# Performance work log

Measured on AMD Instinct MI355X. Metric: run time of the kernel, lower is better.

Reference implementation:

```python
import jax, jax.numpy as jnp
import numpy as np
import math

H = 8  # num_heads

def _gelu(x):
    return jax.nn.gelu(x, approximate=False)

def setup_inputs() -> dict:
    key = jax.random.key(0)
    ks = jax.random.split(key, 16)
    B, N, T, D = 2, 16, 127, 128
    s = 0.02
    inp = {}
    inp["padded_batches"] = jax.random.normal(ks[0], (B, N, T, D), jnp.float32)
    inp["masks"] = jax.random.randint(ks[1], (B, N, T), 0, 2).astype(jnp.int32)
    inp["positions_3d"] = jax.random.normal(ks[2], (B, N, T, 3), jnp.float32)
    inp["Wq"] = jax.random.normal(ks[3], (D, D), jnp.float32) * s
    inp["bq"] = jnp.zeros((D,), jnp.float32)
    inp["Wk"] = jax.random.normal(ks[4], (D, D), jnp.float32) * s
    inp["bk"] = jnp.zeros((D,), jnp.float32)
    inp["Wv"] = jax.random.normal(ks[5], (D, D), jnp.float32) * s
    inp["bv"] = jnp.zeros((D,), jnp.float32)
    inp["gamma"] = jnp.ones((D,), jnp.float32)
    inp["beta"] = jnp.zeros((D,), jnp.float32)
    inp["token_embedding"] = jax.random.normal(ks[6], (1, D), jnp.float32)
    inp["Wb1"] = jax.random.normal(ks[7], (6, 64), jnp.float32) * s
    inp["bb1"] = jnp.zeros((64,), jnp.float32)
    inp["Wb2"] = jax.random.normal(ks[8], (64, H), jnp.float32) * s
    inp["bb2"] = jnp.zeros((H,), jnp.float32)
    inp["Wv1"] = jax.random.normal(ks[9], (6, 128), jnp.float32) * s
    inp["bv1"] = jnp.zeros((128,), jnp.float32)
    inp["Wv2"] = jax.random.normal(ks[10], (128, D), jnp.float32) * s
    inp["bv2"] = jnp.zeros((D,), jnp.float32)
    return inp

def reference(padded_batches, masks, positions_3d, Wq, bq, Wk, bk, Wv, bv, gamma, beta, token_embedding, Wb1, bb1, Wb2, bb2, Wv1, bv1, Wv2, bv2):
    B, N, T, D = padded_batches.shape
    Hd = D // H
    L = T + 1
    scale = 1.0 / math.sqrt(Hd)
    # prepend cls token
    cls = jnp.broadcast_to(token_embedding, (B, N, 1, D))
    x = jnp.concatenate([cls, padded_batches], axis=-2)  # [B,N,L,D]
    q = (x @ Wq + bq).reshape(B * N, L, H, Hd).transpose(0, 2, 1, 3)
    k = (x @ Wk + bk).reshape(B * N, L, H, Hd).transpose(0, 2, 1, 3)
    v = (x @ Wv + bv).reshape(B * N, L, H, Hd).transpose(0, 2, 1, 3)
    keep = jnp.concatenate([jnp.ones((B, N, 1), masks.dtype), masks], axis=-1)
    large_neg = jnp.finfo(jnp.float32).min
    key_mask = jnp.where(keep == 0, large_neg, 0.0).astype(jnp.float32).reshape(B * N, 1, 1, L)
    logits = jnp.einsum('bhid,bhjd->bhij', q, k) * scale
    # relative positional features
    pos = jnp.concatenate([jnp.zeros((B, N, 1, 3), positions_3d.dtype), positions_3d], axis=-2).reshape(B * N, L, 3)
    diff = pos[:, :, None, :] - pos[:, None, :, :]  # [BN,L,L,3]
    dist2 = jnp.sum(diff ** 2, axis=-1, keepdims=True)
    dist = jnp.sqrt(dist2)
    rel_feat = jnp.concatenate([diff, dist, dist, dist2], axis=-1)  # [BN,L,L,6]
    rel_bias = (_gelu(rel_feat @ Wb1 + bb1) @ Wb2 + bb2).transpose(0, 3, 1, 2)  # [BN,H,L,L]
    rel_bias = rel_bias.at[:, :, 0, :].set(0.0).at[:, :, :, 0].set(0.0)
    logits = logits + rel_bias + key_mask
    w = jax.nn.softmax(logits, axis=-1)
    attn = jnp.einsum('bhij,bhjd->bhid', w, v)
    rel_val = (_gelu(rel_feat @ Wv1 + bv1) @ Wv2 + bv2).reshape(B * N, L, L, H, Hd).transpose(0, 3, 1, 2, 4)
    rel_val = rel_val.at[:, :, 0, :, :].set(0.0).at[:, :, :, 0, :].set(0.0)
    attn = attn + jnp.einsum('bhij,bhijc->bhic', w, rel_val)
    attn = attn.transpose(0, 2, 1, 3).reshape(B, N, L, D)
    st = attn[:, :, :1, :] + x[:, :, :1, :]
    mu = jnp.mean(st, axis=-1, keepdims=True)
    var = jnp.var(st, axis=-1, keepdims=True)
    sum_token = (st - mu) / jnp.sqrt(var + 1e-5) * gamma + beta
    out = attn[:, :, 1:, :] + x[:, :, 1:, :]
    return (out, sum_token)
```

## Files before the change

kernel.cpp:

```cpp
#include <hip/hip_runtime.h>
#include <hip/hip_bf16.h>
#include <math.h>

#define BN 32
#define L 128
#define D 128
#define TT 127
#define NH 8

typedef float f32x4 __attribute__((ext_vector_type(4)));
typedef short s16x8 __attribute__((ext_vector_type(8)));

__device__ __forceinline__ float gelu_sig(float x) {
    float e = __expf(-1.702f * x);
    return x * __builtin_amdgcn_rcpf(1.0f + e);
}
__device__ __forceinline__ unsigned short f2bf(float f) {
    unsigned u = __float_as_uint(f);
    return (unsigned short)((u + 0x7fffu + ((u >> 16) & 1u)) >> 16);
}
__device__ __forceinline__ float bf2f(unsigned short v) {
    return __uint_as_float((unsigned)v << 16);
}

__global__ __launch_bounds__(256)
void qkv_bias_kernel(const float* __restrict__ padded, const float* __restrict__ tok,
                     const float* __restrict__ Wq, const float* __restrict__ bq,
                     const float* __restrict__ Wk, const float* __restrict__ bk,
                     const float* __restrict__ Wv, const float* __restrict__ bv,
                     const float* __restrict__ Wb1, const float* __restrict__ bb1,
                     const float* __restrict__ Wb2, const float* __restrict__ bb2,
                     const float* __restrict__ Wv1, const float* __restrict__ bv1,
                     const float* __restrict__ Wv2,
                     const int* __restrict__ masks, const float* __restrict__ pos3d,
                     float* __restrict__ Qo, float* __restrict__ Ko, float* __restrict__ Vo,
                     float* __restrict__ RVW, unsigned short* __restrict__ WV2F,
                     unsigned short* __restrict__ BIAS) {
    const int bid = blockIdx.x;
    const int tid = threadIdx.x;

    if (bid < 384) {
        const int chunk = bid / 96;
        const int rem = bid % 96;
        const int mat = rem >> 5;
        const int s = rem & 31;
        const float* W = (mat == 0) ? Wq : (mat == 1) ? Wk : Wv;
        const float* bias = (mat == 0) ? bq : (mat == 1) ? bk : bv;
        float* outp = (mat == 0) ? Qo : (mat == 1) ? Ko : Vo;

        __shared__ unsigned short Xs[32][136];
        {
            const int row = tid >> 3;
            const int colbase = (tid & 7) * 16;
            const int i = chunk * 32 + row;
            const float* src = (i == 0) ? tok : &padded[(size_t)s * TT * D + (size_t)(i - 1) * D];
#pragma unroll
            for (int k4 = 0; k4 < 4; ++k4) {
                float4 v = *(const float4*)&src[colbase + k4 * 4];
                unsigned lo = (unsigned)f2bf(v.x) | ((unsigned)f2bf(v.y) << 16);
                unsigned hi = (unsigned)f2bf(v.z) | ((unsigned)f2bf(v.w) << 16);
                *(uint2*)&Xs[row][colbase + k4 * 4] = make_uint2(lo, hi);
            }
        }
        __syncthreads();

        const int wave = tid >> 6;
        const int lane = tid & 63;
        const int hA = lane & 15;
        const int kg = lane >> 4;

        s16x8 afr[2][4];
#pragma unroll
        for (int m = 0; m < 2; ++m)
#pragma unroll
            for (int kt = 0; kt < 4; ++kt)
                afr[m][kt] = *(const s16x8*)&Xs[m * 16 + hA][kt * 32 + kg * 8];

        f32x4 acc[2][2];
#pragma unroll
        for (int m = 0; m < 2; ++m)
#pragma unroll
            for (int n = 0; n < 2; ++n) acc[m][n] = (f32x4){0.f, 0.f, 0.f, 0.f};

#pragma unroll
        for (int kt = 0; kt < 4; ++kt) {
#pragma unroll
            for (int n = 0; n < 2; ++n) {
                const int col = (2 * wave + n) * 16 + hA;
                s16x8 bw;
#pragma unroll
                for (int e = 0; e < 8; ++e)
                    bw[e] = (short)f2bf(W[(size_t)(kt * 32 + kg * 8 + e) * D + col]);
                acc[0][n] = __builtin_amdgcn_mfma_f32_16x16x32_bf16(afr[0][kt], bw, acc[0][n], 0, 0, 0);
                acc[1][n] = __builtin_amdgcn_mfma_f32_16x16x32_bf16(afr[1][kt], bw, acc[1][n], 0, 0, 0);
            }
        }

#pragma unroll
        for (int n = 0; n < 2; ++n) {
            const int col = (2 * wave + n) * 16 + hA;
            const float bc = bias[col];
#pragma unroll
            for (int m = 0; m < 2; ++m)
#pragma unroll
                for (int r = 0; r < 4; ++r) {
                    const int row = chunk * 32 + m * 16 + kg * 4 + r;
                    outp[(size_t)s * L * D + (size_t)row * D + col] = acc[m][n][r] + bc;
                }
        }

        if (bid == 0) {
            if (tid < 128) {
                const int cc = tid;
                RVW[cc * 8 + 0] = Wv1[0 * 128 + cc];
                RVW[cc * 8 + 1] = Wv1[1 * 128 + cc];
                RVW[cc * 8 + 2] = Wv1[2 * 128 + cc];
                RVW[cc * 8 + 3] = Wv1[3 * 128 + cc] + Wv1[4 * 128 + cc];
                RVW[cc * 8 + 4] = Wv1[5 * 128 + cc];
                RVW[cc * 8 + 5] = bv1[cc];
                RVW[cc * 8 + 6] = 0.f;
                RVW[cc * 8 + 7] = 0.f;
            }
            for (int idx = tid; idx < 16384; idx += 256) {
                int f = idx >> 9, r = idx & 511, ln = r >> 3, e = r & 7;
                int kt = f >> 3, ng = f & 7;
                int row = kt * 32 + (ln >> 4) * 8 + e;
                int col = ng * 16 + (ln & 15);
                WV2F[idx] = f2bf(Wv2[(size_t)row * D + col]);
            }
        }
    } else {
        const int b2 = bid - 384;
        const int s = b2 >> 6;
        const int jp = b2 & 63;
        const int wv = tid >> 6;
        const int lane = tid & 63;
        const int j = jp * 2 + (wv >> 1);
        const int i = (wv & 1) * 64 + lane;

        if (j == 0) return;
        if (!masks[(size_t)s * TT + (j - 1)]) return;
        const float* pj = pos3d + ((size_t)s * TT + (j - 1)) * 3;
        const int im1 = (i > 0) ? (i - 1) : 0;
        const float* pi = pos3d + ((size_t)s * TT + im1) * 3;
        const float pix = (i > 0) ? pi[0] : 0.f;
        const float piy = (i > 0) ? pi[1] : 0.f;
        const float piz = (i > 0) ? pi[2] : 0.f;
        const float dx = pix - pj[0], dy = piy - pj[1], dz = piz - pj[2];
        const float dist2 = dx * dx + dy * dy + dz * dz;
        const float dist = sqrtf(dist2);

        float bias[NH];
#pragma unroll
        for (int hh = 0; hh < NH; ++hh) bias[hh] = 0.f;
#pragma unroll 2
        for (int u = 0; u < 64; ++u) {
            const float w0 = Wb1[u];
            const float w1 = Wb1[64 + u];
            const float w2 = Wb1[128 + u];
            const float w3 = Wb1[192 + u] + Wb1[256 + u];
            const float w4 = Wb1[320 + u];
            float hv = bb1[u];
            hv = fmaf(dx, w0, hv);
            hv = fmaf(dy, w1, hv);
            hv = fmaf(dz, w2, hv);
            hv = fmaf(dist, w3, hv);
            hv = fmaf(dist2, w4, hv);
            hv = gelu_sig(hv);
            const float* w2p = &Wb2[u * 8];
            bias[0] = fmaf(hv, w2p[0], bias[0]);
            bias[1] = fmaf(hv, w2p[1], bias[1]);
            bias[2] = fmaf(hv, w2p[2], bias[2]);
            bias[3] = fmaf(hv, w2p[3], bias[3]);
            bias[4] = fmaf(hv, w2p[4], bias[4]);
            bias[5] = fmaf(hv, w2p[5], bias[5]);
            bias[6] = fmaf(hv, w2p[6], bias[6]);
            bias[7] = fmaf(hv, w2p[7], bias[7]);
        }
        if (i > 0) {
            uint4 ow;
            ow.x = (unsigned)f2bf(bias[0] + bb2[0]) | ((unsigned)f2bf(bias[1] + bb2[1]) << 16);
            ow.y = (unsigned)f2bf(bias[2] + bb2[2]) | ((unsigned)f2bf(bias[3] + bb2[3]) << 16);
            ow.z = (unsigned)f2bf(bias[4] + bb2[4]) | ((unsigned)f2bf(bias[5] + bb2[5]) << 16);
            ow.w = (unsigned)f2bf(bias[6] + bb2[6]) | ((unsigned)f2bf(bias[7] + bb2[7]) << 16);
            *(uint4*)&BIAS[(((size_t)s * L + i) * L + j) * 8] = ow;
        }
    }
}

__global__ __launch_bounds__(256)
void logits_kernel(const float* __restrict__ Q, const float* __restrict__ K,
                   __hip_bfloat16* __restrict__ LW) {
    const int s = blockIdx.x >> 3;
    const int h = blockIdx.x & 7;
    const int tid = threadIdx.x;
    const int wv = tid >> 6;
    const int lane = tid & 63;
    const int lrn = lane & 15;
    const int kg = lane >> 4;

    __shared__ float Qs[128][16];
    __shared__ float Ks[128][16];
    for (int e = tid; e < 2048; e += 256) {
        int i = e >> 4, d = e & 15;
        Qs[i][d] = Q[((size_t)s * L + i) * D + h * 16 + d];
        Ks[i][d] = K[((size_t)s * L + i) * D + h * 16 + d];
    }
    __syncthreads();

    s16x8 afr[2];
#pragma unroll
    for (int m = 0; m < 2; ++m) {
        s16x8 a;
#pragma unroll
        for (int e = 0; e < 8; ++e) a[e] = 0;
        if (kg < 2) {
            const int i = wv * 32 + m * 16 + lrn;
            float4 q0 = *(const float4*)&Qs[i][kg * 8];
            float4 q1 = *(const float4*)&Qs[i][kg * 8 + 4];
            a[0] = (short)f2bf(q0.x); a[1] = (short)f2bf(q0.y);
            a[2] = (short)f2bf(q0.z); a[3] = (short)f2bf(q0.w);
            a[4] = (short)f2bf(q1.x); a[5] = (short)f2bf(q1.y);
            a[6] = (short)f2bf(q1.z); a[7] = (short)f2bf(q1.w);
        }
        afr[m] = a;
    }

    __hip_bfloat16* lw = LW + ((size_t)(s * NH + h) * L) * L;
#pragma unroll
    for (int n = 0; n < 8; ++n) {
        s16x8 b;
#pragma unroll
        for (int e = 0; e < 8; ++e) b[e] = 0;
        if (kg < 2) {
            const int j = n * 16 + lrn;
            float4 k0 = *(const float4*)&Ks[j][kg * 8];
            float4 k1 = *(const float4*)&Ks[j][kg * 8 + 4];
            b[0] = (short)f2bf(k0.x); b[1] = (short)f2bf(k0.y);
            b[2] = (short)f2bf(k0.z); b[3] = (short)f2bf(k0.w);
            b[4] = (short)f2bf(k1.x); b[5] = (short)f2bf(k1.y);
            b[6] = (short)f2bf(k1.z); b[7] = (short)f2bf(k1.w);
        }
#pragma unroll
        for (int m = 0; m < 2; ++m) {
            f32x4 acc = (f32x4){0.f, 0.f, 0.f, 0.f};
            acc = __builtin_amdgcn_mfma_f32_16x16x32_bf16(afr[m], b, acc, 0, 0, 0);
#pragma unroll
            for (int r = 0; r < 4; ++r)
                lw[(size_t)(wv * 32 + m * 16 + kg * 4 + r) * L + n * 16 + lrn] =
                    __float2bfloat16(acc[r] * 0.25f);
        }
    }
}

__global__ __launch_bounds__(256, 4)
void attn_kernel(const float* __restrict__ padded, const int* __restrict__ masks,
                 const float* __restrict__ pos3d,
                 const float* __restrict__ gamma, const float* __restrict__ beta,
                 const float* __restrict__ tok,
                 const float* __restrict__ RVW,
                 const unsigned short* __restrict__ WV2F,
                 const float* __restrict__ bv2,
                 const float* __restrict__ V, const __hip_bfloat16* __restrict__ LW,
                 const unsigned short* __restrict__ BIAS,
                 float* __restrict__ out) {
    const int i = blockIdx.x;
    const int s = blockIdx.y;
    const int tid = threadIdx.x;
    const int wave = tid >> 6;
    const int lane = tid & 63;
    const int hA = lane & 15;
    const int kg = lane >> 4;
    const int j = tid & 127;
    const int hbase = (tid >> 7) * 4;

    __shared__ float4 feat4_lds[144];
    __shared__ float  feat5_lds[L];
    __shared__ unsigned short w_bf[NH][136];
    __shared__ unsigned short gs_bf[NH][136];
    __shared__ float  a1_part[8][132];
    __shared__ float  a2_lds[D];
    __shared__ float  reds[4][NH];
    __shared__ float  red2[2][2];
    __shared__ unsigned long long kb_lds[2];
    __shared__ int    jmap_lds[128];

    __hip_bfloat16 lr4[4];
#pragma unroll
    for (int k = 0; k < 4; ++k)
        lr4[k] = LW[((size_t)(s * NH + hbase + k) * L + i) * L + j];
    const int keep = (j == 0) ? 1 : masks[(size_t)s * TT + (j - 1)];
    const int ub = (i > 0) && (j > 0) && keep;
    uint2 braw = make_uint2(0u, 0u);
    if (ub) braw = *(const uint2*)&BIAS[(((size_t)s * L + i) * L + j) * 8 + hbase];

    const unsigned long long bal = __ballot(keep != 0);
    if (lane == 0 && wave < 2) kb_lds[wave] = bal;

    if (tid < 128) {
        float pix = 0.f, piy = 0.f, piz = 0.f;
        if (i > 0) { const float* pp = pos3d + ((size_t)s * TT + (i - 1)) * 3; pix = pp[0]; piy = pp[1]; piz = pp[2]; }
        float pjx = 0.f, pjy = 0.f, pjz = 0.f;
        if (tid > 0) { const float* pp = pos3d + ((size_t)s * TT + (tid - 1)) * 3; pjx = pp[0]; pjy = pp[1]; pjz = pp[2]; }
        const float dx = pix - pjx, dy = piy - pjy, dz = piz - pjz;
        const float dist2 = dx * dx + dy * dy + dz * dz;
        const float dist = sqrtf(dist2);
        feat4_lds[tid + (tid >> 3)] = make_float4(dx, dy, dz, dist);
        feat5_lds[tid] = dist2;
        jmap_lds[tid] = 0;
    }
    for (int idx = tid; idx < NH * 68; idx += 256) ((unsigned*)w_bf)[idx] = 0u;
    __syncthreads();

    const unsigned long long b0 = kb_lds[0];
    const int nk = __popcll(b0) + __popcll(kb_lds[1]);
    const int NK32 = (nk + 31) >> 5;
    int rank = 0;
    if (keep) {
        rank = __popcll(bal & ((1ull << lane) - 1)) + ((wave & 1) ? __popcll(b0) : 0);
        if (wave < 2) jmap_lds[rank] = j;
    }

    float badd[4];
    badd[0] = bf2f((unsigned short)(braw.x & 0xffffu));
    badd[1] = bf2f((unsigned short)(braw.x >> 16));
    badd[2] = bf2f((unsigned short)(braw.y & 0xffffu));
    badd[3] = bf2f((unsigned short)(braw.y >> 16));
    float p4[4];
#pragma unroll
    for (int k = 0; k < 4; ++k) {
        float lv = __bfloat162float(lr4[k]) + badd[k];
        p4[k] = keep ? __expf(lv) : 0.f;
    }
#pragma unroll
    for (int k = 0; k < 4; ++k) {
        float v = p4[k];
        for (int off = 32; off >= 1; off >>= 1) v += __shfl_xor(v, off, 64);
        if (lane == 0) reds[wave][hbase + k] = v;
    }
    __syncthreads();
    if (keep) {
        const int pb = (tid >> 7) * 2;
#pragma unroll
        for (int k = 0; k < 4; ++k) {
            const int hh = hbase + k;
            float inv = __builtin_amdgcn_rcpf(reds[pb][hh] + reds[pb + 1][hh]);
            w_bf[hh][rank] = f2bf(p4[k] * inv);
        }
    }
    __syncthreads();

    const int jg = tid >> 5;
    const int c0v = (tid & 31) * 4;
    const int h0v = c0v >> 4;
    const int perg = NK32 * 4;
    const float* Vs = V + (size_t)s * L * D;

    if (i > 0) {
        const int ng0 = 2 * wave;
        float rvw[2][6];
#pragma unroll
        for (int n = 0; n < 2; ++n) {
            const int c = (ng0 + n) * 16 + hA;
            float4 ra = *(const float4*)&RVW[(size_t)c * 8 + 0];
            rvw[n][0] = ra.x; rvw[n][1] = ra.y; rvw[n][2] = ra.z; rvw[n][3] = ra.w;
            rvw[n][4] = RVW[(size_t)c * 8 + 4];
            rvw[n][5] = RVW[(size_t)c * 8 + 5];
        }

        f32x4 accG[2];
#pragma unroll
        for (int n = 0; n < 2; ++n) accG[n] = (f32x4){0.f, 0.f, 0.f, 0.f};

#pragma unroll
        for (int kt = 0; kt < 4; ++kt) {
            if (kt >= NK32) break;
            s16x8 wf;
#pragma unroll
            for (int e = 0; e < 8; ++e) wf[e] = 0;
            if (hA < NH) {
                wf = *(const s16x8*)&w_bf[hA][kt * 32 + kg * 8];
                if (kt == 0 && kg == 0) wf[0] = 0;
            }
            s16x8 bfr[2];
#pragma unroll
            for (int e = 0; e < 8; ++e) {
                const int jj = jmap_lds[kt * 32 + kg * 8 + e];
                float4 fa = feat4_lds[jj + (jj >> 3)];
                float f5 = feat5_lds[jj];
#pragma unroll
                for (int n = 0; n < 2; ++n) {
                    float hv = rvw[n][5];
                    hv = fmaf(fa.x, rvw[n][0], hv);
                    hv = fmaf(fa.y, rvw[n][1], hv);
                    hv = fmaf(fa.z, rvw[n][2], hv);
                    hv = fmaf(fa.w, rvw[n][3], hv);
                    hv = fmaf(f5,  rvw[n][4], hv);
                    bfr[n][e] = (short)f2bf(gelu_sig(hv));
                }
            }
#pragma unroll
            for (int n = 0; n < 2; ++n)
                accG[n] = __builtin_amdgcn_mfma_f32_16x16x32_bf16(wf, bfr[n], accG[n], 0, 0, 0);
        }

        float a1a[4] = {0.f, 0.f, 0.f, 0.f};
        for (int r = 0; r < perg; ++r) {
            const int jt = jg * perg + r;
            const int jr = jmap_lds[jt];
            float4 vcur = *(const float4*)&Vs[(size_t)jr * D + c0v];
            const float wj = bf2f(w_bf[h0v][jt]);
            a1a[0] = fmaf(wj, vcur.x, a1a[0]);
            a1a[1] = fmaf(wj, vcur.y, a1a[1]);
            a1a[2] = fmaf(wj, vcur.z, a1a[2]);
            a1a[3] = fmaf(wj, vcur.w, a1a[3]);
        }
        *(float4*)&a1_part[jg][c0v] = make_float4(a1a[0], a1a[1], a1a[2], a1a[3]);

        if (lane < 32) {
#pragma unroll
            for (int n = 0; n < 2; ++n)
#pragma unroll
                for (int r = 0; r < 4; ++r)
                    gs_bf[(lane >> 4) * 4 + r][(ng0 + n) * 16 + hA] = f2bf(accG[n][r]);
        }
        __syncthreads();

        f32x4 acc2[2];
#pragma unroll
        for (int n = 0; n < 2; ++n) acc2[n] = (f32x4){0.f, 0.f, 0.f, 0.f};
#pragma unroll
        for (int kt = 0; kt < 4; ++kt) {
            s16x8 gf;
#pragma unroll
            for (int e = 0; e < 8; ++e) gf[e] = 0;
            if (hA < NH)
                gf = *(const s16x8*)&gs_bf[hA][kt * 32 + kg * 8];
#pragma unroll
            for (int n = 0; n < 2; ++n) {
                const int f = kt * 8 + ng0 + n;
                s16x8 bw = *(const s16x8*)&WV2F[((size_t)f * 64 + lane) * 8];
                acc2[n] = __builtin_amdgcn_mfma_f32_16x16x32_bf16(gf, bw, acc2[n], 0, 0, 0);
            }
        }
#pragma unroll
        for (int n = 0; n < 2; ++n) {
            const int f = ng0 + n;
            if (kg == (f >> 2)) a2_lds[f * 16 + hA] = acc2[n][f & 3];
        }
        __syncthreads();

        if (tid < 128) {
            float a1f = a1_part[0][tid] + a1_part[1][tid] + a1_part[2][tid] + a1_part[3][tid]
                      + a1_part[4][tid] + a1_part[5][tid] + a1_part[6][tid] + a1_part[7][tid];
            const float S1 = 1.0f - bf2f(w_bf[tid >> 4][0]);
            const size_t o = (size_t)s * TT * D + (size_t)(i - 1) * D + tid;
            out[o] = a1f + a2_lds[tid] + S1 * bv2[tid] + padded[o];
        }
    } else {
        float a1a[4] = {0.f, 0.f, 0.f, 0.f};
        for (int r = 0; r < perg; ++r) {
            const int jt = jg * perg + r;
            const int jr = jmap_lds[jt];
            float4 vcur = *(const float4*)&Vs[(size_t)jr * D + c0v];
            const float wj = bf2f(w_bf[h0v][jt]);
            a1a[0] = fmaf(wj, vcur.x, a1a[0]);
            a1a[1] = fmaf(wj, vcur.y, a1a[1]);
            a1a[2] = fmaf(wj, vcur.z, a1a[2]);
            a1a[3] = fmaf(wj, vcur.w, a1a[3]);
        }
        *(float4*)&a1_part[jg][c0v] = make_float4(a1a[0], a1a[1], a1a[2], a1a[3]);
        __syncthreads();

        float st = 0.f;
        if (tid < 128) {
            float a1f = a1_part[0][tid] + a1_part[1][tid] + a1_part[2][tid] + a1_part[3][tid]
                      + a1_part[4][tid] + a1_part[5][tid] + a1_part[6][tid] + a1_part[7][tid];
            st = a1f + tok[tid];
            float sum = st, sum2 = st * st;
            for (int off = 32; off >= 1; off >>= 1) {
                sum += __shfl_xor(sum, off, 64);
                sum2 += __shfl_xor(sum2, off, 64);
            }
            if (lane == 0) { red2[wave][0] = sum; red2[wave][1] = sum2; }
        }
        __syncthreads();
        if (tid < 128) {
            float sum = red2[0][0] + red2[1][0];
            float sum2 = red2[0][1] + red2[1][1];
            const float mu = sum * (1.0f / 128.0f);
            const float var = sum2 * (1.0f / 128.0f) - mu * mu;
            const float y = (st - mu) * rsqrtf(var + 1e-5f) * gamma[tid] + beta[tid];
            out[(size_t)BN * TT * D + (size_t)s * D + tid] = y;
        }
    }
}

extern "C" void kernel_launch(void* const* d_in, const int* in_sizes, int n_in,
                              void* d_out, int out_size, void* d_ws, size_t ws_size,
                              hipStream_t stream) {
    const float* padded = (const float*)d_in[0];
    const int*   masks  = (const int*)d_in[1];
    const float* pos3d  = (const float*)d_in[2];
    const float* Wq = (const float*)d_in[3];
    const float* bq = (const float*)d_in[4];
    const float* Wk = (const float*)d_in[5];
    const float* bk = (const float*)d_in[6];
    const float* Wv = (const float*)d_in[7];
    const float* bv = (const float*)d_in[8];
    const float* gamma = (const float*)d_in[9];
    const float* beta  = (const float*)d_in[10];
    const float* tok   = (const float*)d_in[11];
    const float* Wb1 = (const float*)d_in[12];
    const float* bb1 = (const float*)d_in[13];
    const float* Wb2 = (const float*)d_in[14];
    const float* bb2 = (const float*)d_in[15];
    const float* Wv1 = (const float*)d_in[16];
    const float* bv1 = (const float*)d_in[17];
    const float* Wv2 = (const float*)d_in[18];
    const float* bv2 = (const float*)d_in[19];
    float* out = (float*)d_out;

    float* Q  = (float*)d_ws;
    float* K  = Q + (size_t)BN * L * D;
    float* Vw = K + (size_t)BN * L * D;
    __hip_bfloat16* LW = (__hip_bfloat16*)(Vw + (size_t)BN * L * D);
    unsigned short* BIAS = (unsigned short*)(LW + (size_t)BN * NH * L * L);
    float* RVW = (float*)(BIAS + (size_t)BN * L * L * NH);
    unsigned short* WV2F = (unsigned short*)(RVW + 128 * 8);

    qkv_bias_kernel<<<dim3(384 + BN * 64), 256, 0, stream>>>(
        padded, tok, Wq, bq, Wk, bk, Wv, bv, Wb1, bb1, Wb2, bb2, Wv1, bv1, Wv2,
        masks, pos3d, Q, K, Vw, RVW, WV2F, BIAS);
    logits_kernel<<<dim3(BN * NH), 256, 0, stream>>>(Q, K, LW);
    attn_kernel<<<dim3(L, BN), 256, 0, stream>>>(padded, masks, pos3d, gamma, beta, tok,
                                                 RVW, WV2F, bv2,
                                                 Vw, LW, BIAS, out);
}
```

Measured before the change: 74.45 us.

## Process two query rows per attention block to share V loads and weights

Each attn_kernel block now handles two query rows (i and i+64) instead of one, which halves the grid. The V-row gather, jmap construction, RVW loads and WV2F fragment loads are shared between the two rows, and the MFMA work for both rows is interleaved. This is meant to cut redundant global traffic and per-block overhead. In exchange it doubles LDS use and register pressure per block, which may lower occupancy, and it leaves fewer blocks in the grid.

```diff
diff --git a/kernel.cpp b/kernel.cpp
--- a/kernel.cpp
+++ b/kernel.cpp
@@ -264,7 +264,7 @@
                  const float* __restrict__ V, const __hip_bfloat16* __restrict__ LW,
                  const unsigned short* __restrict__ BIAS,
                  float* __restrict__ out) {
-    const int i = blockIdx.x;
+    const int bi = blockIdx.x;
     const int s = blockIdx.y;
     const int tid = threadIdx.x;
     const int wave = tid >> 6;
@@ -272,44 +272,53 @@
     const int hA = lane & 15;
     const int kg = lane >> 4;
     const int j = tid & 127;
-    const int hbase = (tid >> 7) * 4;
-
-    __shared__ float4 feat4_lds[144];
-    __shared__ float  feat5_lds[L];
-    __shared__ unsigned short w_bf[NH][136];
-    __shared__ unsigned short gs_bf[NH][136];
-    __shared__ float  a1_part[8][132];
-    __shared__ float  a2_lds[D];
-    __shared__ float  reds[4][NH];
+    const int half = tid >> 7;
+    const int hbase = half * 4;
+    const int i0 = bi, i1 = bi + 64;
+    const int myi = half ? i1 : i0;
+
+    __shared__ float4 feat4_lds[2][144];
+    __shared__ float  feat5_lds[2][128];
+    __shared__ unsigned short w_bf[2][NH][136];
+    __shared__ unsigned short gs_bf[2][NH][136];
+    __shared__ float  a1_part[2][8][132];
+    __shared__ float  a2_lds[2][D];
+    __shared__ float  reds[2][4][NH];
     __shared__ float  red2[2][2];
     __shared__ unsigned long long kb_lds[2];
     __shared__ int    jmap_lds[128];
 
-    __hip_bfloat16 lr4[4];
-#pragma unroll
-    for (int k = 0; k < 4; ++k)
-        lr4[k] = LW[((size_t)(s * NH + hbase + k) * L + i) * L + j];
+    __hip_bfloat16 lr[2][4];
+#pragma unroll
+    for (int k = 0; k < 4; ++k) {
+        lr[0][k] = LW[((size_t)(s * NH + hbase + k) * L + i0) * L + j];
+        lr[1][k] = LW[((size_t)(s * NH + hbase + k) * L + i1) * L + j];
+    }
     const int keep = (j == 0) ? 1 : masks[(size_t)s * TT + (j - 1)];
-    const int ub = (i > 0) && (j > 0) && keep;
-    uint2 braw = make_uint2(0u, 0u);
-    if (ub) braw = *(const uint2*)&BIAS[(((size_t)s * L + i) * L + j) * 8 + hbase];
+    uint2 braw[2];
+    braw[0] = make_uint2(0u, 0u);
+    braw[1] = make_uint2(0u, 0u);
+    if ((j > 0) && keep) {
+        if (i0 > 0) braw[0] = *(const uint2*)&BIAS[(((size_t)s * L + i0) * L + j) * 8 + hbase];
+        braw[1] = *(const uint2*)&BIAS[(((size_t)s * L + i1) * L + j) * 8 + hbase];
+    }
 
     const unsigned long long bal = __ballot(keep != 0);
     if (lane == 0 && wave < 2) kb_lds[wave] = bal;
 
-    if (tid < 128) {
+    {
         float pix = 0.f, piy = 0.f, piz = 0.f;
-        if (i > 0) { const float* pp = pos3d + ((size_t)s * TT + (i - 1)) * 3; pix = pp[0]; piy = pp[1]; piz = pp[2]; }
+        if (myi > 0) { const float* pp = pos3d + ((size_t)s * TT + (myi - 1)) * 3; pix = pp[0]; piy = pp[1]; piz = pp[2]; }
         float pjx = 0.f, pjy = 0.f, pjz = 0.f;
-        if (tid > 0) { const float* pp = pos3d + ((size_t)s * TT + (tid - 1)) * 3; pjx = pp[0]; pjy = pp[1]; pjz = pp[2]; }
+        if (j > 0) { const float* pp = pos3d + ((size_t)s * TT + (j - 1)) * 3; pjx = pp[0]; pjy = pp[1]; pjz = pp[2]; }
         const float dx = pix - pjx, dy = piy - pjy, dz = piz - pjz;
         const float dist2 = dx * dx + dy * dy + dz * dz;
         const float dist = sqrtf(dist2);
-        feat4_lds[tid + (tid >> 3)] = make_float4(dx, dy, dz, dist);
-        feat5_lds[tid] = dist2;
-        jmap_lds[tid] = 0;
-    }
-    for (int idx = tid; idx < NH * 68; idx += 256) ((unsigned*)w_bf)[idx] = 0u;
+        feat4_lds[half][j + (j >> 3)] = make_float4(dx, dy, dz, dist);
+        feat5_lds[half][j] = dist2;
+        if (half == 0) jmap_lds[j] = 0;
+    }
+    for (int idx = tid; idx < 2 * NH * 68; idx += 256) ((unsigned*)w_bf)[idx] = 0u;
     __syncthreads();
 
     const unsigned long long b0 = kb_lds[0];
@@ -321,32 +330,39 @@
         if (wave < 2) jmap_lds[rank] = j;
     }
 
-    float badd[4];
-    badd[0] = bf2f((unsigned short)(braw.x & 0xffffu));
-    badd[1] = bf2f((unsigned short)(braw.x >> 16));
-    badd[2] = bf2f((unsigned short)(braw.y & 0xffffu));
-    badd[3] = bf2f((unsigned short)(braw.y >> 16));
-    float p4[4];
-#pragma unroll
-    for (int k = 0; k < 4; ++k) {
-        float lv = __bfloat162float(lr4[k]) + badd[k];
-        p4[k] = keep ? __expf(lv) : 0.f;
-    }
-#pragma unroll
-    for (int k = 0; k < 4; ++k) {
-        float v = p4[k];
-        for (int off = 32; off >= 1; off >>= 1) v += __shfl_xor(v, off, 64);
-        if (lane == 0) reds[wave][hbase + k] = v;
-    }
+    float p[2][4];
+#pragma unroll
+    for (int i2 = 0; i2 < 2; ++i2) {
+        float badd[4];
+        badd[0] = bf2f((unsigned short)(braw[i2].x & 0xffffu));
+        badd[1] = bf2f((unsigned short)(braw[i2].x >> 16));
+        badd[2] = bf2f((unsigned short)(braw[i2].y & 0xffffu));
+        badd[3] = bf2f((unsigned short)(braw[i2].y >> 16));
+#pragma unroll
+        for (int k = 0; k < 4; ++k) {
+            float lv = __bfloat162float(lr[i2][k]) + badd[k];
+            p[i2][k] = keep ? __expf(lv) : 0.f;
+        }
+    }
+#pragma unroll
+    for (int i2 = 0; i2 < 2; ++i2)
+#pragma unroll
+        for (int k = 0; k < 4; ++k) {
+            float v = p[i2][k];
+            for (int off = 32; off >= 1; off >>= 1) v += __shfl_xor(v, off, 64);
+            if (lane == 0) reds[i2][wave][hbase + k] = v;
+        }
     __syncthreads();
     if (keep) {
-        const int pb = (tid >> 7) * 2;
-#pragma unroll
-        for (int k = 0; k < 4; ++k) {
-            const int hh = hbase + k;
-            float inv = __builtin_amdgcn_rcpf(reds[pb][hh] + reds[pb + 1][hh]);
-            w_bf[hh][rank] = f2bf(p4[k] * inv);
-        }
+        const int pb = half * 2;
+#pragma unroll
+        for (int i2 = 0; i2 < 2; ++i2)
+#pragma unroll
+            for (int k = 0; k < 4; ++k) {
+                const int hh = hbase + k;
+                float inv = __builtin_amdgcn_rcpf(reds[i2][pb][hh] + reds[i2][pb + 1][hh]);
+                w_bf[i2][hh][rank] = f2bf(p[i2][k] * inv);
+            }
     }
     __syncthreads();
 
@@ -355,39 +371,47 @@
     const int h0v = c0v >> 4;
     const int perg = NK32 * 4;
     const float* Vs = V + (size_t)s * L * D;
-
-    if (i > 0) {
-        const int ng0 = 2 * wave;
-        float rvw[2][6];
-#pragma unroll
-        for (int n = 0; n < 2; ++n) {
-            const int c = (ng0 + n) * 16 + hA;
-            float4 ra = *(const float4*)&RVW[(size_t)c * 8 + 0];
-            rvw[n][0] = ra.x; rvw[n][1] = ra.y; rvw[n][2] = ra.z; rvw[n][3] = ra.w;
-            rvw[n][4] = RVW[(size_t)c * 8 + 4];
-            rvw[n][5] = RVW[(size_t)c * 8 + 5];
-        }
-
-        f32x4 accG[2];
-#pragma unroll
-        for (int n = 0; n < 2; ++n) accG[n] = (f32x4){0.f, 0.f, 0.f, 0.f};
-
-#pragma unroll
-        for (int kt = 0; kt < 4; ++kt) {
-            if (kt >= NK32) break;
-            s16x8 wf;
-#pragma unroll
-            for (int e = 0; e < 8; ++e) wf[e] = 0;
-            if (hA < NH) {
-                wf = *(const s16x8*)&w_bf[hA][kt * 32 + kg * 8];
-                if (kt == 0 && kg == 0) wf[0] = 0;
-            }
-            s16x8 bfr[2];
-#pragma unroll
-            for (int e = 0; e < 8; ++e) {
-                const int jj = jmap_lds[kt * 32 + kg * 8 + e];
-                float4 fa = feat4_lds[jj + (jj >> 3)];
-                float f5 = feat5_lds[jj];
+    const int istart = (i0 == 0) ? 1 : 0;
+    const int ng0 = 2 * wave;
+
+    float rvw[2][6];
+#pragma unroll
+    for (int n = 0; n < 2; ++n) {
+        const int c = (ng0 + n) * 16 + hA;
+        float4 ra = *(const float4*)&RVW[(size_t)c * 8 + 0];
+        rvw[n][0] = ra.x; rvw[n][1] = ra.y; rvw[n][2] = ra.z; rvw[n][3] = ra.w;
+        rvw[n][4] = RVW[(size_t)c * 8 + 4];
+        rvw[n][5] = RVW[(size_t)c * 8 + 5];
+    }
+
+    f32x4 accG[2][2];
+#pragma unroll
+    for (int i2 = 0; i2 < 2; ++i2)
+#pragma unroll
+        for (int n = 0; n < 2; ++n) accG[i2][n] = (f32x4){0.f, 0.f, 0.f, 0.f};
+
+#pragma unroll
+    for (int kt = 0; kt < 4; ++kt) {
+        if (kt >= NK32) break;
+        s16x8 wf[2];
+#pragma unroll
+        for (int i2 = 0; i2 < 2; ++i2) {
+#pragma unroll
+            for (int e = 0; e < 8; ++e) wf[i2][e] = 0;
+            if (hA < NH && i2 >= istart) {
+                wf[i2] = *(const s16x8*)&w_bf[i2][hA][kt * 32 + kg * 8];
+                if (kt == 0 && kg == 0) wf[i2][0] = 0;
+            }
+        }
+        s16x8 bfr[2][2];
+#pragma unroll
+        for (int e = 0; e < 8; ++e) {
+            const int jj = jmap_lds[kt * 32 + kg * 8 + e];
+#pragma unroll
+            for (int i2 = 0; i2 < 2; ++i2) {
+                if (i2 < istart) continue;
+                float4 fa = feat4_lds[i2][jj + (jj >> 3)];
+                float f5 = feat5_lds[i2][jj];
 #pragma unroll
                 for (int n = 0; n < 2; ++n) {
                     float hv = rvw[n][5];
@@ -396,87 +420,109 @@
                     hv = fmaf(fa.z, rvw[n][2], hv);
                     hv = fmaf(fa.w, rvw[n][3], hv);
                     hv = fmaf(f5,  rvw[n][4], hv);
-                    bfr[n][e] = (short)f2bf(gelu_sig(hv));
+                    bfr[i2][n][e] = (short)f2bf(gelu_sig(hv));
                 }
             }
+        }
+#pragma unroll
+        for (int i2 = 0; i2 < 2; ++i2) {
+            if (i2 < istart) continue;
 #pragma unroll
             for (int n = 0; n < 2; ++n)
-                accG[n] = __builtin_amdgcn_mfma_f32_16x16x32_bf16(wf, bfr[n], accG[n], 0, 0, 0);
-        }
-
-        float a1a[4] = {0.f, 0.f, 0.f, 0.f};
+                accG[i2][n] = __builtin_amdgcn_mfma_f32_16x16x32_bf16(wf[i2], bfr[i2][n], accG[i2][n], 0, 0, 0);
+        }
+    }
+
+    {
+        float a10[4] = {0.f, 0.f, 0.f, 0.f};
+        float a11[4] = {0.f, 0.f, 0.f, 0.f};
         for (int r = 0; r < perg; ++r) {
             const int jt = jg * perg + r;
             const int jr = jmap_lds[jt];
             float4 vcur = *(const float4*)&Vs[(size_t)jr * D + c0v];
-            const float wj = bf2f(w_bf[h0v][jt]);
-            a1a[0] = fmaf(wj, vcur.x, a1a[0]);
-            a1a[1] = fmaf(wj, vcur.y, a1a[1]);
-            a1a[2] = fmaf(wj, vcur.z, a1a[2]);
-            a1a[3] = fmaf(wj, vcur.w, a1a[3]);
-        }
-        *(float4*)&a1_part[jg][c0v] = make_float4(a1a[0], a1a[1], a1a[2], a1a[3]);
-
-        if (lane < 32) {
+            const float w0 = bf2f(w_bf[0][h0v][jt]);
+            const float w1 = bf2f(w_bf[1][h0v][jt]);
+            a10[0] = fmaf(w0, vcur.x, a10[0]);
+            a10[1] = fmaf(w0, vcur.y, a10[1]);
+            a10[2] = fmaf(w0, vcur.z, a10[2]);
+            a10[3] = fmaf(w0, vcur.w, a10[3]);
+            a11[0] = fmaf(w1, vcur.x, a11[0]);
+            a11[1] = fmaf(w1, vcur.y, a11[1]);
+            a11[2] = fmaf(w1, vcur.z, a11[2]);
+            a11[3] = fmaf(w1, vcur.w, a11[3]);
+        }
+        *(float4*)&a1_part[0][jg][c0v] = make_float4(a10[0], a10[1], a10[2], a10[3]);
+        *(float4*)&a1_part[1][jg][c0v] = make_float4(a11[0], a11[1], a11[2], a11[3]);
+    }
+
+    if (lane < 32) {
+#pragma unroll
+        for (int i2 = 0; i2 < 2; ++i2) {
+            if (i2 < istart) continue;
 #pragma unroll
             for (int n = 0; n < 2; ++n)
 #pragma unroll
                 for (int r = 0; r < 4; ++r)
-                    gs_bf[(lane >> 4) * 4 + r][(ng0 + n) * 16 + hA] = f2bf(accG[n][r]);
-        }
-        __syncthreads();
-
-        f32x4 acc2[2];
-#pragma unroll
-        for (int n = 0; n < 2; ++n) acc2[n] = (f32x4){0.f, 0.f, 0.f, 0.f};
-#pragma unroll
-        for (int kt = 0; kt < 4; ++kt) {
-            s16x8 gf;
-#pragma unroll
-            for (int e = 0; e < 8; ++e) gf[e] = 0;
-            if (hA < NH)
-                gf = *(const s16x8*)&gs_bf[hA][kt * 32 + kg * 8];
-#pragma unroll
-            for (int n = 0; n < 2; ++n) {
-                const int f = kt * 8 + ng0 + n;
-                s16x8 bw = *(const s16x8*)&WV2F[((size_t)f * 64 + lane) * 8];
-                acc2[n] = __builtin_amdgcn_mfma_f32_16x16x32_bf16(gf, bw, acc2[n], 0, 0, 0);
-            }
+                    gs_bf[i2][(lane >> 4) * 4 + r][(ng0 + n) * 16 + hA] = f2bf(accG[i2][n][r]);
+        }
+    }
+    __syncthreads();
+
+    f32x4 acc2[2][2];
+#pragma unroll
+    for (int i2 = 0; i2 < 2; ++i2)
+#pragma unroll
+        for (int n = 0; n < 2; ++n) acc2[i2][n] = (f32x4){0.f, 0.f, 0.f, 0.f};
+#pragma unroll
+    for (int kt = 0; kt < 4; ++kt) {
+        s16x8 gf[2];
+#pragma unroll
+        for (int i2 = 0; i2 < 2; ++i2) {
+#pragma unroll
+            for (int e = 0; e < 8; ++e) gf[i2][e] = 0;
+            if (hA < NH && i2 >= istart)
+                gf[i2] = *(const s16x8*)&gs_bf[i2][hA][kt * 32 + kg * 8];
         }
 #pragma unroll
         for (int n = 0; n < 2; ++n) {
-            const int f = ng0 + n;
-            if (kg == (f >> 2)) a2_lds[f * 16 + hA] = acc2[n][f & 3];
-        }
-        __syncthreads();
-
-        if (tid < 128) {
-            float a1f = a1_part[0][tid] + a1_part[1][tid] + a1_part[2][tid] + a1_part[3][tid]
-                      + a1_part[4][tid] + a1_part[5][tid] + a1_part[6][tid] + a1_part[7][tid];
-            const float S1 = 1.0f - bf2f(w_bf[tid >> 4][0]);
-            const size_t o = (size_t)s * TT * D + (size_t)(i - 1) * D + tid;
-            out[o] = a1f + a2_lds[tid] + S1 * bv2[tid] + padded[o];
-        }
+            const int f = kt * 8 + ng0 + n;
+            s16x8 bw = *(const s16x8*)&WV2F[((size_t)f * 64 + lane) * 8];
+#pragma unroll
+            for (int i2 = 0; i2 < 2; ++i2) {
+                if (i2 < istart) continue;
+                acc2[i2][n] = __builtin_amdgcn_mfma_f32_16x16x32_bf16(gf[i2], bw, acc2[i2][n], 0, 0, 0);
+            }
+        }
+    }
+#pragma unroll
+    for (int n = 0; n < 2; ++n) {
+        const int f = ng0 + n;
+        if (kg == (f >> 2)) {
+#pragma unroll
+            for (int i2 = 0; i2 < 2; ++i2) {
+                if (i2 < istart) continue;
+                a2_lds[i2][f * 16 + hA] = acc2[i2][n][f & 3];
+            }
+        }
+    }
+    __syncthreads();
+
+    float a1f = a1_part[half][0][j] + a1_part[half][1][j] + a1_part[half][2][j] + a1_part[half][3][j]
+              + a1_part[half][4][j] + a1_part[half][5][j] + a1_part[half][6][j] + a1_part[half][7][j];
+
+    if (i0 > 0) {
+        const float S1 = 1.0f - bf2f(w_bf[half][j >> 4][0]);
+        const size_t o = (size_t)s * TT * D + (size_t)(myi - 1) * D + j;
+        out[o] = a1f + a2_lds[half][j] + S1 * bv2[j] + padded[o];
     } else {
-        float a1a[4] = {0.f, 0.f, 0.f, 0.f};
-        for (int r = 0; r < perg; ++r) {
-            const int jt = jg * perg + r;
-            const int jr = jmap_lds[jt];
-            float4 vcur = *(const float4*)&Vs[(size_t)jr * D + c0v];
-            const float wj = bf2f(w_bf[h0v][jt]);
-            a1a[0] = fmaf(wj, vcur.x, a1a[0]);
-            a1a[1] = fmaf(wj, vcur.y, a1a[1]);
-            a1a[2] = fmaf(wj, vcur.z, a1a[2]);
-            a1a[3] = fmaf(wj, vcur.w, a1a[3]);
-        }
-        *(float4*)&a1_part[jg][c0v] = make_float4(a1a[0], a1a[1], a1a[2], a1a[3]);
-        __syncthreads();
-
+        if (half == 1) {
+            const float S1 = 1.0f - bf2f(w_bf[1][j >> 4][0]);
+            const size_t o = (size_t)s * TT * D + (size_t)(i1 - 1) * D + j;
+            out[o] = a1f + a2_lds[1][j] + S1 * bv2[j] + padded[o];
+        }
         float st = 0.f;
-        if (tid < 128) {
-            float a1f = a1_part[0][tid] + a1_part[1][tid] + a1_part[2][tid] + a1_part[3][tid]
-                      + a1_part[4][tid] + a1_part[5][tid] + a1_part[6][tid] + a1_part[7][tid];
-            st = a1f + tok[tid];
+        if (half == 0) {
+            st = a1f + tok[j];
             float sum = st, sum2 = st * st;
             for (int off = 32; off >= 1; off >>= 1) {
                 sum += __shfl_xor(sum, off, 64);
@@ -485,13 +531,13 @@
             if (lane == 0) { red2[wave][0] = sum; red2[wave][1] = sum2; }
         }
         __syncthreads();
-        if (tid < 128) {
+        if (half == 0) {
             float sum = red2[0][0] + red2[1][0];
             float sum2 = red2[0][1] + red2[1][1];
             const float mu = sum * (1.0f / 128.0f);
             const float var = sum2 * (1.0f / 128.0f) - mu * mu;
-            const float y = (st - mu) * rsqrtf(var + 1e-5f) * gamma[tid] + beta[tid];
-            out[(size_t)BN * TT * D + (size_t)s * D + tid] = y;
+            const float y = (st - mu) * rsqrtf(var + 1e-5f) * gamma[j] + beta[j];
+            out[(size_t)BN * TT * D + (size_t)s * D + j] = y;
         }
     }
 }
@@ -533,7 +579,7 @@
         padded, tok, Wq, bq, Wk, bk, Wv, bv, Wb1, bb1, Wb2, bb2, Wv1, bv1, Wv2,
         masks, pos3d, Q, K, Vw, RVW, WV2F, BIAS);
     logits_kernel<<<dim3(BN * NH), 256, 0, stream>>>(Q, K, LW);
-    attn_kernel<<<dim3(L, BN), 256, 0, stream>>>(padded, masks, pos3d, gamma, beta, tok,
-                                                 RVW, WV2F, bv2,
-                                                 Vw, LW, BIAS, out);
-}
+    attn_kernel<<<dim3(L / 2, BN), 256, 0, stream>>>(padded, masks, pos3d, gamma, beta, tok,
+                                                     RVW, WV2F, bv2,
+                                                     Vw, LW, BIAS, out);
+}
```

Measured after the change: 75.52 us. No clear change (+1.4%).

## Store V as bf16 MFMA fragments and compute attn·V with MFMA

Applied to the files above, without the earlier changes.

The V projection is now written as bf16 in a pre-swizzled MFMA B-fragment layout instead of fp32 row-major. The attention kernel keeps an unpacked copy of the softmax weights indexed by key position and computes w·V with 16x16x32 bf16 MFMAs over all 128 keys. This replaces the scalar FMA gather loop over compacted kept keys and its 8-way partial-sum reduction. It halves V memory traffic and removes the LDS partial buffer, but it does dense work over masked keys and adds bf16 rounding of V.

```diff
diff --git a/kernel.cpp b/kernel.cpp
--- a/kernel.cpp
+++ b/kernel.cpp
@@ -33,7 +33,8 @@
                      const float* __restrict__ Wv1, const float* __restrict__ bv1,
                      const float* __restrict__ Wv2,
                      const int* __restrict__ masks, const float* __restrict__ pos3d,
-                     float* __restrict__ Qo, float* __restrict__ Ko, float* __restrict__ Vo,
+                     float* __restrict__ Qo, float* __restrict__ Ko,
+                     unsigned short* __restrict__ VF,
                      float* __restrict__ RVW, unsigned short* __restrict__ WV2F,
                      unsigned short* __restrict__ BIAS) {
     const int bid = blockIdx.x;
@@ -46,7 +47,7 @@
         const int s = rem & 31;
         const float* W = (mat == 0) ? Wq : (mat == 1) ? Wk : Wv;
         const float* bias = (mat == 0) ? bq : (mat == 1) ? bk : bv;
-        float* outp = (mat == 0) ? Qo : (mat == 1) ? Ko : Vo;
+        float* outp = (mat == 0) ? Qo : Ko;
 
         __shared__ unsigned short Xs[32][136];
         {
@@ -96,17 +97,42 @@
             }
         }
 
-#pragma unroll
-        for (int n = 0; n < 2; ++n) {
-            const int col = (2 * wave + n) * 16 + hA;
-            const float bc = bias[col];
-#pragma unroll
-            for (int m = 0; m < 2; ++m)
-#pragma unroll
-                for (int r = 0; r < 4; ++r) {
-                    const int row = chunk * 32 + m * 16 + kg * 4 + r;
-                    outp[(size_t)s * L * D + (size_t)row * D + col] = acc[m][n][r] + bc;
-                }
+        if (mat != 2) {
+#pragma unroll
+            for (int n = 0; n < 2; ++n) {
+                const int col = (2 * wave + n) * 16 + hA;
+                const float bc = bias[col];
+#pragma unroll
+                for (int m = 0; m < 2; ++m)
+#pragma unroll
+                    for (int r = 0; r < 4; ++r) {
+                        const int row = chunk * 32 + m * 16 + kg * 4 + r;
+                        outp[(size_t)s * L * D + (size_t)row * D + col] = acc[m][n][r] + bc;
+                    }
+            }
+        } else {
+            __syncthreads();
+#pragma unroll
+            for (int n = 0; n < 2; ++n) {
+                const int col = (2 * wave + n) * 16 + hA;
+                const float bc = bias[col];
+#pragma unroll
+                for (int m = 0; m < 2; ++m)
+#pragma unroll
+                    for (int r = 0; r < 4; ++r)
+                        Xs[m * 16 + kg * 4 + r][col] = f2bf(acc[m][n][r] + bc);
+            }
+            __syncthreads();
+#pragma unroll
+            for (int pass = 0; pass < 2; ++pass) {
+                const int idx = pass * 256 + tid;
+                const int fl = idx >> 6, ln = idx & 63;
+                unsigned short v8[8];
+#pragma unroll
+                for (int e = 0; e < 8; ++e)
+                    v8[e] = Xs[(ln >> 4) * 8 + e][fl * 16 + (ln & 15)];
+                *(uint4*)&VF[(size_t)s * 16384 + ((size_t)(chunk * 8 + fl) * 64 + ln) * 8] = *(uint4*)v8;
+            }
         }
 
         if (bid == 0) {
@@ -261,7 +287,7 @@
                  const float* __restrict__ RVW,
                  const unsigned short* __restrict__ WV2F,
                  const float* __restrict__ bv2,
-                 const float* __restrict__ V, const __hip_bfloat16* __restrict__ LW,
+                 const unsigned short* __restrict__ VF, const __hip_bfloat16* __restrict__ LW,
                  const unsigned short* __restrict__ BIAS,
                  float* __restrict__ out) {
     const int i = blockIdx.x;
@@ -277,9 +303,9 @@
     __shared__ float4 feat4_lds[144];
     __shared__ float  feat5_lds[L];
     __shared__ unsigned short w_bf[NH][136];
+    __shared__ unsigned short wu_bf[NH][136];
     __shared__ unsigned short gs_bf[NH][136];
-    __shared__ float  a1_part[8][132];
-    __shared__ float  a2_lds[D];
+    __shared__ float  a12_lds[2][D];
     __shared__ float  reds[4][NH];
     __shared__ float  red2[2][2];
     __shared__ unsigned long long kb_lds[2];
@@ -309,7 +335,10 @@
         feat5_lds[tid] = dist2;
         jmap_lds[tid] = 0;
     }
-    for (int idx = tid; idx < NH * 68; idx += 256) ((unsigned*)w_bf)[idx] = 0u;
+    for (int idx = tid; idx < NH * 68; idx += 256) {
+        ((unsigned*)w_bf)[idx] = 0u;
+        ((unsigned*)wu_bf)[idx] = 0u;
+    }
     __syncthreads();
 
     const unsigned long long b0 = kb_lds[0];
@@ -345,19 +374,40 @@
         for (int k = 0; k < 4; ++k) {
             const int hh = hbase + k;
             float inv = __builtin_amdgcn_rcpf(reds[pb][hh] + reds[pb + 1][hh]);
-            w_bf[hh][rank] = f2bf(p4[k] * inv);
+            unsigned short wn = f2bf(p4[k] * inv);
+            w_bf[hh][rank] = wn;
+            wu_bf[hh][j] = wn;
         }
     }
     __syncthreads();
 
-    const int jg = tid >> 5;
-    const int c0v = (tid & 31) * 4;
-    const int h0v = c0v >> 4;
-    const int perg = NK32 * 4;
-    const float* Vs = V + (size_t)s * L * D;
+    const int ng0 = 2 * wave;
+    const unsigned short* VFs = VF + (size_t)s * 16384;
+
+    f32x4 acc1[2];
+    acc1[0] = (f32x4){0.f, 0.f, 0.f, 0.f};
+    acc1[1] = (f32x4){0.f, 0.f, 0.f, 0.f};
+#pragma unroll
+    for (int kt = 0; kt < 4; ++kt) {
+        s16x8 wuf;
+#pragma unroll
+        for (int e = 0; e < 8; ++e) wuf[e] = 0;
+        if (hA < NH)
+            wuf = *(const s16x8*)&wu_bf[hA][kt * 32 + kg * 8];
+#pragma unroll
+        for (int n = 0; n < 2; ++n) {
+            const int f = kt * 8 + ng0 + n;
+            s16x8 bw = *(const s16x8*)&VFs[((size_t)f * 64 + lane) * 8];
+            acc1[n] = __builtin_amdgcn_mfma_f32_16x16x32_bf16(wuf, bw, acc1[n], 0, 0, 0);
+        }
+    }
+#pragma unroll
+    for (int n = 0; n < 2; ++n) {
+        const int f = ng0 + n;
+        if (kg == (f >> 2)) a12_lds[0][f * 16 + hA] = acc1[n][f & 3];
+    }
 
     if (i > 0) {
-        const int ng0 = 2 * wave;
         float rvw[2][6];
 #pragma unroll
         for (int n = 0; n < 2; ++n) {
@@ -404,19 +454,6 @@
                 accG[n] = __builtin_amdgcn_mfma_f32_16x16x32_bf16(wf, bfr[n], accG[n], 0, 0, 0);
         }
 
-        float a1a[4] = {0.f, 0.f, 0.f, 0.f};
-        for (int r = 0; r < perg; ++r) {
-            const int jt = jg * perg + r;
-            const int jr = jmap_lds[jt];
-            float4 vcur = *(const float4*)&Vs[(size_t)jr * D + c0v];
-            const float wj = bf2f(w_bf[h0v][jt]);
-            a1a[0] = fmaf(wj, vcur.x, a1a[0]);
-            a1a[1] = fmaf(wj, vcur.y, a1a[1]);
-            a1a[2] = fmaf(wj, vcur.z, a1a[2]);
-            a1a[3] = fmaf(wj, vcur.w, a1a[3]);
-        }
-        *(float4*)&a1_part[jg][c0v] = make_float4(a1a[0], a1a[1], a1a[2], a1a[3]);
-
         if (lane < 32) {
 #pragma unroll
             for (int n = 0; n < 2; ++n)
@@ -446,37 +483,21 @@
 #pragma unroll
         for (int n = 0; n < 2; ++n) {
             const int f = ng0 + n;
-            if (kg == (f >> 2)) a2_lds[f * 16 + hA] = acc2[n][f & 3];
+            if (kg == (f >> 2)) a12_lds[1][f * 16 + hA] = acc2[n][f & 3];
         }
         __syncthreads();
 
         if (tid < 128) {
-            float a1f = a1_part[0][tid] + a1_part[1][tid] + a1_part[2][tid] + a1_part[3][tid]
-                      + a1_part[4][tid] + a1_part[5][tid] + a1_part[6][tid] + a1_part[7][tid];
-            const float S1 = 1.0f - bf2f(w_bf[tid >> 4][0]);
+            const float S1 = 1.0f - bf2f(wu_bf[tid >> 4][0]);
             const size_t o = (size_t)s * TT * D + (size_t)(i - 1) * D + tid;
-            out[o] = a1f + a2_lds[tid] + S1 * bv2[tid] + padded[o];
+            out[o] = a12_lds[0][tid] + a12_lds[1][tid] + S1 * bv2[tid] + padded[o];
         }
     } else {
-        float a1a[4] = {0.f, 0.f, 0.f, 0.f};
-        for (int r = 0; r < perg; ++r) {
-            const int jt = jg * perg + r;
-            const int jr = jmap_lds[jt];
-            float4 vcur = *(const float4*)&Vs[(size_t)jr * D + c0v];
-            const float wj = bf2f(w_bf[h0v][jt]);
-            a1a[0] = fmaf(wj, vcur.x, a1a[0]);
-            a1a[1] = fmaf(wj, vcur.y, a1a[1]);
-            a1a[2] = fmaf(wj, vcur.z, a1a[2]);
-            a1a[3] = fmaf(wj, vcur.w, a1a[3]);
-        }
-        *(float4*)&a1_part[jg][c0v] = make_float4(a1a[0], a1a[1], a1a[2], a1a[3]);
         __syncthreads();
 
         float st = 0.f;
         if (tid < 128) {
-            float a1f = a1_part[0][tid] + a1_part[1][tid] + a1_part[2][tid] + a1_part[3][tid]
-                      + a1_part[4][tid] + a1_part[5][tid] + a1_part[6][tid] + a1_part[7][tid];
-            st = a1f + tok[tid];
+            st = a12_lds[0][tid] + tok[tid];
             float sum = st, sum2 = st * st;
             for (int off = 32; off >= 1; off >>= 1) {
                 sum += __shfl_xor(sum, off, 64);
@@ -523,17 +544,17 @@
 
     float* Q  = (float*)d_ws;
     float* K  = Q + (size_t)BN * L * D;
-    float* Vw = K + (size_t)BN * L * D;
-    __hip_bfloat16* LW = (__hip_bfloat16*)(Vw + (size_t)BN * L * D);
+    unsigned short* VF = (unsigned short*)(K + (size_t)BN * L * D);
+    __hip_bfloat16* LW = (__hip_bfloat16*)(VF + (size_t)BN * L * D);
     unsigned short* BIAS = (unsigned short*)(LW + (size_t)BN * NH * L * L);
     float* RVW = (float*)(BIAS + (size_t)BN * L * L * NH);
     unsigned short* WV2F = (unsigned short*)(RVW + 128 * 8);
 
     qkv_bias_kernel<<<dim3(384 + BN * 64), 256, 0, stream>>>(
         padded, tok, Wq, bq, Wk, bk, Wv, bv, Wb1, bb1, Wb2, bb2, Wv1, bv1, Wv2,
-        masks, pos3d, Q, K, Vw, RVW, WV2F, BIAS);
+        masks, pos3d, Q, K, VF, RVW, WV2F, BIAS);
     logits_kernel<<<dim3(BN * NH), 256, 0, stream>>>(Q, K, LW);
     attn_kernel<<<dim3(L, BN), 256, 0, stream>>>(padded, masks, pos3d, gamma, beta, tok,
                                                  RVW, WV2F, bv2,
-                                                 Vw, LW, BIAS, out);
-}
+                                                 VF, LW, BIAS, out);
+}
```

After: 76.02 us. 1.02x slower.
